# Performance work log

Measured on AMD Instinct MI355X. Metric: run time of the kernel, lower is better.

Reference implementation:

```python
import jax, jax.numpy as jnp
import numpy as np

N_RULES = 64  # R
OUT_PER_RULE = 64  # O, fc out = R*O = 4096


def setup_inputs() -> dict:
    key = jax.random.key(0)
    k1, k2, k3, k4 = jax.random.split(key, 4)
    S, D_IN = 8192, 1024
    RO = N_RULES * OUT_PER_RULE
    X = jax.random.normal(k1, (S, D_IN), dtype=jnp.float32)
    # torch.nn.Linear-style weight [out, in] and bias [out]
    W = jax.random.normal(k2, (RO, D_IN), dtype=jnp.float32) * (1.0 / np.sqrt(D_IN))
    b = jax.random.normal(k3, (RO,), dtype=jnp.float32) * 0.01
    # rule firing strengths (computed under no_grad in the original)
    lambdas = jax.random.uniform(k4, (S, N_RULES), dtype=jnp.float32)
    return {"X": X, "W": W, "b": b, "lambdas": lambdas}


def reference(X, W, b, lambdas):
    # fc + sigmoid: [S, R*O]
    H = jax.nn.sigmoid(X @ W.T + b)
    S = H.shape[0]
    # apply_rule_strength: block-diagonal lambda_eye @ H^T is exactly a
    # rule-weighted sum over the R consecutive O-sized blocks of H.
    Hr = H.reshape(S, N_RULES, OUT_PER_RULE)  # [S, R, O]
    Y = jnp.einsum("sr,sro->so", lambdas, Hr)  # [S, O]
    return Y
```

## Files before the change

### kernel.cpp

```cpp
#include <hip/hip_runtime.h>

#define S_DIM 8192
#define K_DIM 1024
#define RO_DIM 4096
#define O_DIM 64
#define SO (S_DIM * O_DIM)
#define NSLICE 16

typedef __attribute__((ext_vector_type(8))) __bf16 bf16x8;
typedef __attribute__((ext_vector_type(4))) float floatx4;
typedef __attribute__((ext_vector_type(4))) unsigned short ushx4;
typedef __attribute__((ext_vector_type(8))) unsigned short ushx8;

__device__ inline unsigned short f2bf(float f) {
  unsigned u = __builtin_bit_cast(unsigned, f);
  u += 0x7fff + ((u >> 16) & 1);
  return (unsigned short)(u >> 16);
}
__device__ inline float bf2f(unsigned short h) {
  unsigned u = ((unsigned)h) << 16;
  return __builtin_bit_cast(float, u);
}

__global__ __launch_bounds__(256) void cast_kernel(const float* __restrict__ X,
                                                   const float* __restrict__ W,
                                                   unsigned short* __restrict__ Xb,
                                                   unsigned short* __restrict__ Wb) {
  const int NX4 = (S_DIM * K_DIM) / 4;
#pragma unroll
  for (int i = 0; i < 4; ++i) {
    int g = blockIdx.x * 1024 + i * 256 + threadIdx.x;
    float4 v;
    unsigned short* dst;
    if (g < NX4) {
      v = ((const float4*)X)[g];
      dst = Xb + (size_t)g * 4;
    } else {
      int j = g - NX4;
      v = ((const float4*)W)[j];
      dst = Wb + (size_t)j * 4;
    }
    ushx4 o;
    o.x = f2bf(v.x); o.y = f2bf(v.y); o.z = f2bf(v.z); o.w = f2bf(v.w);
    *(ushx4*)dst = o;
  }
}


template <int MB, int NB>
__device__ __forceinline__ void mfmaq(floatx4 (&acc)[8][4], const bf16x8 (&afr)[4][2],
                                      const bf16x8 (&bfr)[4][2]) {
  __builtin_amdgcn_s_setprio(1);
#pragma unroll
  for (int ks = 0; ks < 2; ++ks)
#pragma unroll
    for (int m = 0; m < 4; ++m)
#pragma unroll
      for (int n = 0; n < 2; ++n)
        acc[MB + m][NB + n] = __builtin_amdgcn_mfma_f32_16x16x32_bf16(
            afr[m][ks], bfr[NB + n][ks], acc[MB + m][NB + n], 0, 0, 0);
  __builtin_amdgcn_s_setprio(0);
}

#define BAR() __builtin_amdgcn_s_barrier()

__global__ __launch_bounds__(512, 2) void gemm_kernel(const unsigned short* __restrict__ Xb,
                                                      const unsigned short* __restrict__ Wb,
                                                      const float* __restrict__ bias,
                                                      const float* __restrict__ lam,
                                                      unsigned short* __restrict__ partial) {
  __shared__ __align__(16) unsigned char smem[135168];
  unsigned short* sm = (unsigned short*)smem;
  float* lamsh = (float*)(smem + 131072);

  const int t = threadIdx.x;
  const int lane = t & 63;
  const int w = t >> 6;
  const int wm = w >> 2;
  const int wn = w & 3;
  const int quad = lane >> 4;
  const int l16 = lane & 15;

  int id = blockIdx.y * 16 + blockIdx.x;
  int x = id & 7;
  int j = id >> 3;
  const int bx = 2 * x + (j & 1);
  const int by = j >> 1;
  const int gm0 = by * 256;
  const int gn0 = bx * 256;

  const int rowt = t >> 3;
  const int gcc = (t & 7) ^ (rowt & 7);
  const size_t goff = (size_t)rowt * K_DIM + (size_t)gcc * 8;
  const unsigned short* Abase = Xb + (size_t)gm0 * K_DIM;
  const unsigned short* Bbase = Wb + (size_t)gn0 * K_DIM;

  auto STAGE = [&](const unsigned short* gbase, int half, int ktile, int slotOff) {
#pragma unroll
    for (int jj = 0; jj < 2; ++jj) {
      const unsigned short* src =
          gbase + (size_t)(half * 128 + jj * 64) * K_DIM + ktile * 64 + goff;
      __builtin_amdgcn_global_load_lds(
          (const __attribute__((address_space(1))) void*)src,
          (__attribute__((address_space(3))) void*)(sm + slotOff + jj * 4096 + t * 8),
          16, 0, 0);
    }
  };

  STAGE(Abase, 0, 0, 0);
  STAGE(Abase, 1, 0, 8192);
  STAGE(Bbase, 0, 0, 16384);
  STAGE(Bbase, 1, 0, 24576);
  STAGE(Bbase, 0, 1, 32768 + 16384);
  STAGE(Bbase, 1, 1, 32768 + 24576);
  STAGE(Abase, 0, 1, 32768 + 0);

  {
    int i = t;
    lamsh[i] = lam[(size_t)(gm0 + (i >> 2)) * 64 + bx * 4 + (i & 3)];
    i = t + 512;
    lamsh[i] = lam[(size_t)(gm0 + (i >> 2)) * 64 + bx * 4 + (i & 3)];
  }
  asm volatile("s_waitcnt vmcnt(6)" ::: "memory");
  BAR();

  floatx4 acc[8][4];
#pragma unroll
  for (int ni = 0; ni < 4; ++ni) {
    float bv = bias[gn0 + wn * 64 + ni * 16 + l16];
#pragma unroll
    for (int mi = 0; mi < 8; ++mi) acc[mi][ni] = (floatx4){bv, bv, bv, bv};
  }

  const int cA0 = ((quad) ^ (l16 & 7)) * 8;
  const int cA1 = ((4 + quad) ^ (l16 & 7)) * 8;

  for (int kt = 0; kt < 16; ++kt) {
    const int b = kt & 1;
    const unsigned short* As = sm + b * 32768 + wm * 8192 + l16 * 64;
    const unsigned short* Bs = sm + b * 32768 + 16384 + wn * 4096 + l16 * 64;
    const int bufN = (b ^ 1) * 32768;
    const int bufC = b * 32768;

    bf16x8 afr[4][2], bfr[4][2];

#pragma unroll
    for (int m = 0; m < 4; ++m) {
      afr[m][0] = *(const bf16x8*)(As + m * 1024 + cA0);
      afr[m][1] = *(const bf16x8*)(As + m * 1024 + cA1);
    }
#pragma unroll
    for (int n = 0; n < 2; ++n) {
      bfr[n][0] = *(const bf16x8*)(Bs + n * 1024 + cA0);
      bfr[n][1] = *(const bf16x8*)(Bs + n * 1024 + cA1);
    }
    if (kt < 15) STAGE(Abase, 1, kt + 1, bufN + 8192);
    BAR();
    mfmaq<0, 0>(acc, afr, bfr);
    BAR();

#pragma unroll
    for (int n = 2; n < 4; ++n) {
      bfr[n][0] = *(const bf16x8*)(Bs + n * 1024 + cA0);
      bfr[n][1] = *(const bf16x8*)(Bs + n * 1024 + cA1);
    }
    BAR();
    mfmaq<0, 2>(acc, afr, bfr);
    BAR();

#pragma unroll
    for (int m = 0; m < 4; ++m) {
      afr[m][0] = *(const bf16x8*)(As + (4 + m) * 1024 + cA0);
      afr[m][1] = *(const bf16x8*)(As + (4 + m) * 1024 + cA1);
    }
    if (kt < 14) STAGE(Bbase, 0, kt + 2, bufC + 16384);
    BAR();
    mfmaq<4, 0>(acc, afr, bfr);
    BAR();

    if (kt < 14) {
      STAGE(Bbase, 1, kt + 2, bufC + 24576);
      STAGE(Abase, 0, kt + 2, bufC + 0);
    }
    mfmaq<4, 2>(acc, afr, bfr);
    if (kt < 14) {
      asm volatile("s_waitcnt vmcnt(6)" ::: "memory");
    } else if (kt == 14) {
      asm volatile("s_waitcnt vmcnt(0)" ::: "memory");
    }
    BAR();
  }

  __syncthreads();
  {
    unsigned short* yreg = sm + wn * 16384;
#pragma unroll
    for (int mi = 0; mi < 8; ++mi) {
#pragma unroll
      for (int r = 0; r < 4; ++r) {
        int row = wm * 128 + mi * 16 + quad * 4 + r;
        float lamv = lamsh[row * 4 + wn];
#pragma unroll
        for (int ni = 0; ni < 4; ++ni) {
          float sg = 1.f / (1.f + __expf(-acc[mi][ni][r]));
          yreg[row * 64 + ((ni ^ quad) * 16) + l16] = f2bf(lamv * sg);
        }
      }
    }
  }
  __syncthreads();
  {
    unsigned short* pb = partial + (size_t)bx * SO + (size_t)gm0 * 64;
#pragma unroll
    for (int g = 0; g < 4; ++g) {
      int idx = g * 4096 + t * 8;
      int row = idx >> 6;
      int c = idx & 63;
      int phys = row * 64 + ((((c >> 4) ^ ((row >> 2) & 3))) << 4) + (c & 15);
      float s[8];
#pragma unroll
      for (int jj = 0; jj < 8; ++jj) s[jj] = 0.f;
#pragma unroll
      for (int q = 0; q < 4; ++q) {
        ushx8 v = *(const ushx8*)(sm + q * 16384 + phys);
#pragma unroll
        for (int jj = 0; jj < 8; ++jj) s[jj] += bf2f(v[jj]);
      }
      ushx8 o;
#pragma unroll
      for (int jj = 0; jj < 8; ++jj) o[jj] = f2bf(s[jj]);
      *(ushx8*)(pb + idx) = o;
    }
  }
}

__global__ __launch_bounds__(256) void reduce_kernel(const unsigned short* __restrict__ partial,
                                                     float* __restrict__ Y) {
  int i4 = blockIdx.x * 256 + threadIdx.x;
  float s0 = 0.f, s1 = 0.f, s2 = 0.f, s3 = 0.f;
#pragma unroll
  for (int c = 0; c < NSLICE; ++c) {
    ushx4 v = ((const ushx4*)(partial + (size_t)c * SO))[i4];
    s0 += bf2f(v.x); s1 += bf2f(v.y); s2 += bf2f(v.z); s3 += bf2f(v.w);
  }
  ((float4*)Y)[i4] = (float4){s0, s1, s2, s3};
}

extern "C" void kernel_launch(void* const* d_in, const int* in_sizes, int n_in,
                              void* d_out, int out_size, void* d_ws, size_t ws_size,
                              hipStream_t stream) {
  const float* X = (const float*)d_in[0];
  const float* W = (const float*)d_in[1];
  const float* b = (const float*)d_in[2];
  const float* lam = (const float*)d_in[3];
  float* Y = (float*)d_out;

  unsigned short* Xb = (unsigned short*)d_ws;
  unsigned short* Wb = Xb + (size_t)S_DIM * K_DIM;
  unsigned short* partial = Wb + (size_t)RO_DIM * K_DIM;

  int nCast = ((S_DIM + RO_DIM) * K_DIM / 4) / 1024;
  cast_kernel<<<nCast, 256, 0, stream>>>(X, W, Xb, Wb);

  dim3 g(RO_DIM / 256, S_DIM / 256);
  gemm_kernel<<<g, 512, 0, stream>>>(Xb, Wb, b, lam, partial);

  reduce_kernel<<<SO / 1024, 256, 0, stream>>>(partial, Y);
}
```

Measured before the change: 168.6 us.

## Prefetch next k-tile register fragments during final MFMA quadrant

Splits the A and B register fragments into separate double-buffered sets (af0/af1, bf01/bf23). The first A half and B columns 0-1 of the next k-tile are now read from LDS before the last MFMA quadrant of the current tile, and the global-to-LDS stage issues are regrouped around the quadrants. The aim is to hide LDS read latency behind MFMA work. In exchange it holds more live VGPRs under a 512-thread, 2-blocks-per-CU launch bound. It also reads the next buffer right after the waitcnt with no barrier first, so other threads' LDS writes may not be visible yet, and it adds one barrier per iteration.

```diff
diff --git a/kernel.cpp b/kernel.cpp
--- a/kernel.cpp
+++ b/kernel.cpp
@@ -48,8 +48,8 @@
 
 
 template <int MB, int NB>
-__device__ __forceinline__ void mfmaq(floatx4 (&acc)[8][4], const bf16x8 (&afr)[4][2],
-                                      const bf16x8 (&bfr)[4][2]) {
+__device__ __forceinline__ void mfmaq(floatx4 (&acc)[8][4], const bf16x8 (&af)[4][2],
+                                      const bf16x8 (&bf)[2][2]) {
   __builtin_amdgcn_s_setprio(1);
 #pragma unroll
   for (int ks = 0; ks < 2; ++ks)
@@ -58,8 +58,25 @@
 #pragma unroll
       for (int n = 0; n < 2; ++n)
         acc[MB + m][NB + n] = __builtin_amdgcn_mfma_f32_16x16x32_bf16(
-            afr[m][ks], bfr[NB + n][ks], acc[MB + m][NB + n], 0, 0, 0);
+            af[m][ks], bf[n][ks], acc[MB + m][NB + n], 0, 0, 0);
   __builtin_amdgcn_s_setprio(0);
+}
+
+__device__ __forceinline__ void rdA(bf16x8 (&af)[4][2], const unsigned short* As,
+                                    int mbase, int cA0, int cA1) {
+#pragma unroll
+  for (int m = 0; m < 4; ++m) {
+    af[m][0] = *(const bf16x8*)(As + (mbase + m) * 1024 + cA0);
+    af[m][1] = *(const bf16x8*)(As + (mbase + m) * 1024 + cA1);
+  }
+}
+__device__ __forceinline__ void rdB(bf16x8 (&bf)[2][2], const unsigned short* Bs,
+                                    int nbase, int cA0, int cA1) {
+#pragma unroll
+  for (int n = 0; n < 2; ++n) {
+    bf[n][0] = *(const bf16x8*)(Bs + (nbase + n) * 1024 + cA0);
+    bf[n][1] = *(const bf16x8*)(Bs + (nbase + n) * 1024 + cA1);
+  }
 }
 
 #define BAR() __builtin_amdgcn_s_barrier()
@@ -135,59 +152,52 @@
   const int cA0 = ((quad) ^ (l16 & 7)) * 8;
   const int cA1 = ((4 + quad) ^ (l16 & 7)) * 8;
 
+  const int Aoff = wm * 8192 + l16 * 64;
+  const int Boff = 16384 + wn * 4096 + l16 * 64;
+
+  bf16x8 af0[4][2], af1[4][2], bf01[2][2], bf23[2][2];
+
+  rdA(af0, sm + Aoff, 0, cA0, cA1);
+  rdB(bf01, sm + Boff, 0, cA0, cA1);
+
   for (int kt = 0; kt < 16; ++kt) {
     const int b = kt & 1;
-    const unsigned short* As = sm + b * 32768 + wm * 8192 + l16 * 64;
-    const unsigned short* Bs = sm + b * 32768 + 16384 + wn * 4096 + l16 * 64;
+    const unsigned short* As = sm + b * 32768 + Aoff;
+    const unsigned short* Bs = sm + b * 32768 + Boff;
+    const unsigned short* AsN = sm + (b ^ 1) * 32768 + Aoff;
+    const unsigned short* BsN = sm + (b ^ 1) * 32768 + Boff;
     const int bufN = (b ^ 1) * 32768;
     const int bufC = b * 32768;
 
-    bf16x8 afr[4][2], bfr[4][2];
-
-#pragma unroll
-    for (int m = 0; m < 4; ++m) {
-      afr[m][0] = *(const bf16x8*)(As + m * 1024 + cA0);
-      afr[m][1] = *(const bf16x8*)(As + m * 1024 + cA1);
-    }
-#pragma unroll
-    for (int n = 0; n < 2; ++n) {
-      bfr[n][0] = *(const bf16x8*)(Bs + n * 1024 + cA0);
-      bfr[n][1] = *(const bf16x8*)(Bs + n * 1024 + cA1);
-    }
+    rdB(bf23, Bs, 2, cA0, cA1);
     if (kt < 15) STAGE(Abase, 1, kt + 1, bufN + 8192);
     BAR();
-    mfmaq<0, 0>(acc, afr, bfr);
-    BAR();
-
-#pragma unroll
-    for (int n = 2; n < 4; ++n) {
-      bfr[n][0] = *(const bf16x8*)(Bs + n * 1024 + cA0);
-      bfr[n][1] = *(const bf16x8*)(Bs + n * 1024 + cA1);
-    }
-    BAR();
-    mfmaq<0, 2>(acc, afr, bfr);
-    BAR();
-
-#pragma unroll
-    for (int m = 0; m < 4; ++m) {
-      afr[m][0] = *(const bf16x8*)(As + (4 + m) * 1024 + cA0);
-      afr[m][1] = *(const bf16x8*)(As + (4 + m) * 1024 + cA1);
-    }
+    mfmaq<0, 0>(acc, af0, bf01);
+    BAR();
+
+    rdA(af1, As, 4, cA0, cA1);
     if (kt < 14) STAGE(Bbase, 0, kt + 2, bufC + 16384);
     BAR();
-    mfmaq<4, 0>(acc, afr, bfr);
+    mfmaq<0, 2>(acc, af0, bf23);
+    BAR();
+
+    if (kt < 14) STAGE(Bbase, 1, kt + 2, bufC + 24576);
+    BAR();
+    mfmaq<4, 0>(acc, af1, bf01);
     BAR();
 
     if (kt < 14) {
-      STAGE(Bbase, 1, kt + 2, bufC + 24576);
       STAGE(Abase, 0, kt + 2, bufC + 0);
-    }
-    mfmaq<4, 2>(acc, afr, bfr);
-    if (kt < 14) {
       asm volatile("s_waitcnt vmcnt(6)" ::: "memory");
     } else if (kt == 14) {
       asm volatile("s_waitcnt vmcnt(0)" ::: "memory");
     }
+    if (kt < 15) {
+      rdA(af0, AsN, 0, cA0, cA1);
+      rdB(bf01, BsN, 0, cA0, cA1);
+    }
+    BAR();
+    mfmaq<4, 2>(acc, af1, bf23);
     BAR();
   }
 
```

Result: no change. 166.3 us (-1.4%).

## Fuse fp32-to-bf16 cast into GEMM via register-staged loads

Applied to the files above, without the earlier changes.

Removes the separate cast kernel and makes the GEMM read fp32 X and W directly. Each tile is loaded into registers, converted with v_cvt_pk_bf16_f32, and written to LDS, replacing direct global-to-LDS loads. This saves the bf16 intermediate round trip and one launch. In exchange it doubles global read bytes per tile, since X and W are re-read as fp32 across tiles, and adds register pressure from the in-flight load sets. The pipeline now relies on the compiler's implicit vmcnt waits.

```diff
diff --git a/kernel.cpp b/kernel.cpp
--- a/kernel.cpp
+++ b/kernel.cpp
@@ -22,34 +22,16 @@
   return __builtin_bit_cast(float, u);
 }
 
-__global__ __launch_bounds__(256) void cast_kernel(const float* __restrict__ X,
-                                                   const float* __restrict__ W,
-                                                   unsigned short* __restrict__ Xb,
-                                                   unsigned short* __restrict__ Wb) {
-  const int NX4 = (S_DIM * K_DIM) / 4;
-#pragma unroll
-  for (int i = 0; i < 4; ++i) {
-    int g = blockIdx.x * 1024 + i * 256 + threadIdx.x;
-    float4 v;
-    unsigned short* dst;
-    if (g < NX4) {
-      v = ((const float4*)X)[g];
-      dst = Xb + (size_t)g * 4;
-    } else {
-      int j = g - NX4;
-      v = ((const float4*)W)[j];
-      dst = Wb + (size_t)j * 4;
-    }
-    ushx4 o;
-    o.x = f2bf(v.x); o.y = f2bf(v.y); o.z = f2bf(v.z); o.w = f2bf(v.w);
-    *(ushx4*)dst = o;
-  }
+__device__ __forceinline__ unsigned cvtpk(float lo, float hi) {
+  unsigned r;
+  asm("v_cvt_pk_bf16_f32 %0, %1, %2" : "=v"(r) : "v"(lo), "v"(hi));
+  return r;
 }
 
 
 template <int MB, int NB>
-__device__ __forceinline__ void mfmaq(floatx4 (&acc)[8][4], const bf16x8 (&afr)[4][2],
-                                      const bf16x8 (&bfr)[4][2]) {
+__device__ __forceinline__ void mfmaq(floatx4 (&acc)[8][4], const bf16x8 (&af)[4][2],
+                                      const bf16x8 (&bf)[4][2]) {
   __builtin_amdgcn_s_setprio(1);
 #pragma unroll
   for (int ks = 0; ks < 2; ++ks)
@@ -58,14 +40,16 @@
 #pragma unroll
       for (int n = 0; n < 2; ++n)
         acc[MB + m][NB + n] = __builtin_amdgcn_mfma_f32_16x16x32_bf16(
-            afr[m][ks], bfr[NB + n][ks], acc[MB + m][NB + n], 0, 0, 0);
+            af[m][ks], bf[NB + n][ks], acc[MB + m][NB + n], 0, 0, 0);
   __builtin_amdgcn_s_setprio(0);
 }
 
+struct ldset { float4 a, b, c, d; };
+
 #define BAR() __builtin_amdgcn_s_barrier()
 
-__global__ __launch_bounds__(512, 2) void gemm_kernel(const unsigned short* __restrict__ Xb,
-                                                      const unsigned short* __restrict__ Wb,
+__global__ __launch_bounds__(512, 2) void gemm_kernel(const float* __restrict__ X,
+                                                      const float* __restrict__ W,
                                                       const float* __restrict__ bias,
                                                       const float* __restrict__ lam,
                                                       unsigned short* __restrict__ partial) {
@@ -91,29 +75,35 @@
 
   const int rowt = t >> 3;
   const int gcc = (t & 7) ^ (rowt & 7);
-  const size_t goff = (size_t)rowt * K_DIM + (size_t)gcc * 8;
-  const unsigned short* Abase = Xb + (size_t)gm0 * K_DIM;
-  const unsigned short* Bbase = Wb + (size_t)gn0 * K_DIM;
-
-  auto STAGE = [&](const unsigned short* gbase, int half, int ktile, int slotOff) {
-#pragma unroll
-    for (int jj = 0; jj < 2; ++jj) {
-      const unsigned short* src =
-          gbase + (size_t)(half * 128 + jj * 64) * K_DIM + ktile * 64 + goff;
-      __builtin_amdgcn_global_load_lds(
-          (const __attribute__((address_space(1))) void*)src,
-          (__attribute__((address_space(3))) void*)(sm + slotOff + jj * 4096 + t * 8),
-          16, 0, 0);
-    }
+  const size_t goffE = (size_t)rowt * K_DIM + (size_t)gcc * 8;
+  const float* Asrc = X + (size_t)gm0 * K_DIM;
+  const float* Bsrc = W + (size_t)gn0 * K_DIM;
+
+  auto LDht = [&](ldset& h, const float* gb, int half, int ktile) {
+    const float* p0 = gb + (size_t)(half * 128) * K_DIM + ktile * 64 + goffE;
+    const float* p1 = p0 + (size_t)64 * K_DIM;
+    h.a = *(const float4*)p0; h.b = *(const float4*)(p0 + 4);
+    h.c = *(const float4*)p1; h.d = *(const float4*)(p1 + 4);
   };
-
-  STAGE(Abase, 0, 0, 0);
-  STAGE(Abase, 1, 0, 8192);
-  STAGE(Bbase, 0, 0, 16384);
-  STAGE(Bbase, 1, 0, 24576);
-  STAGE(Bbase, 0, 1, 32768 + 16384);
-  STAGE(Bbase, 1, 1, 32768 + 24576);
-  STAGE(Abase, 0, 1, 32768 + 0);
+  auto WRht = [&](const ldset& h, int slotOff) {
+    uint4 w0, w1;
+    w0.x = cvtpk(h.a.x, h.a.y); w0.y = cvtpk(h.a.z, h.a.w);
+    w0.z = cvtpk(h.b.x, h.b.y); w0.w = cvtpk(h.b.z, h.b.w);
+    w1.x = cvtpk(h.c.x, h.c.y); w1.y = cvtpk(h.c.z, h.c.w);
+    w1.z = cvtpk(h.d.x, h.d.y); w1.w = cvtpk(h.d.z, h.d.w);
+    *(uint4*)(sm + slotOff + t * 8) = w0;
+    *(uint4*)(sm + slotOff + 4096 + t * 8) = w1;
+  };
+
+  {
+    ldset u, v;
+    LDht(u, Asrc, 0, 0); LDht(v, Asrc, 1, 0); WRht(u, 0);              WRht(v, 8192);
+    LDht(u, Bsrc, 0, 0); LDht(v, Bsrc, 1, 0); WRht(u, 16384);          WRht(v, 24576);
+    LDht(u, Bsrc, 0, 1); LDht(v, Bsrc, 1, 1); WRht(u, 32768 + 16384);  WRht(v, 32768 + 24576);
+    LDht(u, Asrc, 0, 1); WRht(u, 32768 + 0);
+  }
+  ldset ldA1, ldB0, ldB1, ldA0;
+  LDht(ldA1, Asrc, 1, 1);
 
   {
     int i = t;
@@ -121,7 +111,7 @@
     i = t + 512;
     lamsh[i] = lam[(size_t)(gm0 + (i >> 2)) * 64 + bx * 4 + (i & 3)];
   }
-  asm volatile("s_waitcnt vmcnt(6)" ::: "memory");
+  asm volatile("s_waitcnt lgkmcnt(0)" ::: "memory");
   BAR();
 
   floatx4 acc[8][4];
@@ -154,9 +144,10 @@
       bfr[n][0] = *(const bf16x8*)(Bs + n * 1024 + cA0);
       bfr[n][1] = *(const bf16x8*)(Bs + n * 1024 + cA1);
     }
-    if (kt < 15) STAGE(Abase, 1, kt + 1, bufN + 8192);
+    if (kt < 15) WRht(ldA1, bufN + 8192);
     BAR();
     mfmaq<0, 0>(acc, afr, bfr);
+    if (kt < 14) LDht(ldB0, Bsrc, 0, kt + 2);
     BAR();
 
 #pragma unroll
@@ -166,6 +157,7 @@
     }
     BAR();
     mfmaq<0, 2>(acc, afr, bfr);
+    if (kt < 14) LDht(ldB1, Bsrc, 1, kt + 2);
     BAR();
 
 #pragma unroll
@@ -173,21 +165,19 @@
       afr[m][0] = *(const bf16x8*)(As + (4 + m) * 1024 + cA0);
       afr[m][1] = *(const bf16x8*)(As + (4 + m) * 1024 + cA1);
     }
-    if (kt < 14) STAGE(Bbase, 0, kt + 2, bufC + 16384);
+    if (kt < 14) WRht(ldB0, bufC + 16384);
     BAR();
     mfmaq<4, 0>(acc, afr, bfr);
+    if (kt < 14) LDht(ldA0, Asrc, 0, kt + 2);
     BAR();
 
     if (kt < 14) {
-      STAGE(Bbase, 1, kt + 2, bufC + 24576);
-      STAGE(Abase, 0, kt + 2, bufC + 0);
+      WRht(ldB1, bufC + 24576);
+      WRht(ldA0, bufC + 0);
     }
     mfmaq<4, 2>(acc, afr, bfr);
-    if (kt < 14) {
-      asm volatile("s_waitcnt vmcnt(6)" ::: "memory");
-    } else if (kt == 14) {
-      asm volatile("s_waitcnt vmcnt(0)" ::: "memory");
-    }
+    if (kt < 14) LDht(ldA1, Asrc, 1, kt + 2);
+    asm volatile("s_waitcnt lgkmcnt(0)" ::: "memory");
     BAR();
   }
 
@@ -255,15 +245,10 @@
   const float* lam = (const float*)d_in[3];
   float* Y = (float*)d_out;
 
-  unsigned short* Xb = (unsigned short*)d_ws;
-  unsigned short* Wb = Xb + (size_t)S_DIM * K_DIM;
-  unsigned short* partial = Wb + (size_t)RO_DIM * K_DIM;
-
-  int nCast = ((S_DIM + RO_DIM) * K_DIM / 4) / 1024;
-  cast_kernel<<<nCast, 256, 0, stream>>>(X, W, Xb, Wb);
+  unsigned short* partial = (unsigned short*)d_ws;
 
   dim3 g(RO_DIM / 256, S_DIM / 256);
-  gemm_kernel<<<g, 512, 0, stream>>>(Xb, Wb, b, lam, partial);
+  gemm_kernel<<<g, 512, 0, stream>>>(X, W, b, lam, partial);
 
   reduce_kernel<<<SO / 1024, 256, 0, stream>>>(partial, Y);
 }
```

After: 188.0 us. +11.5%, slower.

## Fuse slice reduction into GEMM via last-block atomic counter

Applied to the files above, without the earlier changes.

Removes the separate reduce kernel. Each GEMM block increments a per-row-block atomic counter after writing its bf16 partial, and the last of the 16 column blocks sums all slices for its 256 rows and writes Y directly. This saves one kernel launch and lets the reduction overlap with other blocks' GEMM work, at the cost of an added memset, thread fences, and serialized tail work in the last block per row group.

```diff
diff --git a/kernel.cpp b/kernel.cpp
--- a/kernel.cpp
+++ b/kernel.cpp
@@ -68,8 +68,11 @@
                                                       const unsigned short* __restrict__ Wb,
                                                       const float* __restrict__ bias,
                                                       const float* __restrict__ lam,
-                                                      unsigned short* __restrict__ partial) {
+                                                      unsigned short* __restrict__ partial,
+                                                      int* __restrict__ ctr,
+                                                      float* __restrict__ Y) {
   __shared__ __align__(16) unsigned char smem[135168];
+  __shared__ int lastFlag;
   unsigned short* sm = (unsigned short*)smem;
   float* lamsh = (float*)(smem + 131072);
 
@@ -232,18 +235,33 @@
       *(ushx8*)(pb + idx) = o;
     }
   }
-}
-
-__global__ __launch_bounds__(256) void reduce_kernel(const unsigned short* __restrict__ partial,
-                                                     float* __restrict__ Y) {
-  int i4 = blockIdx.x * 256 + threadIdx.x;
-  float s0 = 0.f, s1 = 0.f, s2 = 0.f, s3 = 0.f;
-#pragma unroll
-  for (int c = 0; c < NSLICE; ++c) {
-    ushx4 v = ((const ushx4*)(partial + (size_t)c * SO))[i4];
-    s0 += bf2f(v.x); s1 += bf2f(v.y); s2 += bf2f(v.z); s3 += bf2f(v.w);
-  }
-  ((float4*)Y)[i4] = (float4){s0, s1, s2, s3};
+
+  __syncthreads();
+  if (t == 0) {
+    __threadfence();
+    lastFlag = (atomicAdd(&ctr[by], 1) == NSLICE - 1);
+  }
+  __syncthreads();
+  if (lastFlag) {
+    __threadfence();
+    const unsigned short* pb0 = partial + (size_t)gm0 * 64;
+    float* Yb = Y + (size_t)gm0 * 64;
+#pragma unroll
+    for (int g = 0; g < 4; ++g) {
+      int idx = g * 4096 + t * 8;
+      float s[8];
+#pragma unroll
+      for (int jj = 0; jj < 8; ++jj) s[jj] = 0.f;
+#pragma unroll 4
+      for (int sl = 0; sl < NSLICE; ++sl) {
+        ushx8 v = *(const ushx8*)(pb0 + (size_t)sl * SO + idx);
+#pragma unroll
+        for (int jj = 0; jj < 8; ++jj) s[jj] += bf2f(v[jj]);
+      }
+      *(float4*)(Yb + idx) = (float4){s[0], s[1], s[2], s[3]};
+      *(float4*)(Yb + idx + 4) = (float4){s[4], s[5], s[6], s[7]};
+    }
+  }
 }
 
 extern "C" void kernel_launch(void* const* d_in, const int* in_sizes, int n_in,
@@ -258,12 +276,13 @@
   unsigned short* Xb = (unsigned short*)d_ws;
   unsigned short* Wb = Xb + (size_t)S_DIM * K_DIM;
   unsigned short* partial = Wb + (size_t)RO_DIM * K_DIM;
+  int* ctr = (int*)(partial + (size_t)NSLICE * SO);
+
+  hipMemsetAsync(ctr, 0, 32 * sizeof(int), stream);
 
   int nCast = ((S_DIM + RO_DIM) * K_DIM / 4) / 1024;
   cast_kernel<<<nCast, 256, 0, stream>>>(X, W, Xb, Wb);
 
   dim3 g(RO_DIM / 256, S_DIM / 256);
-  gemm_kernel<<<g, 512, 0, stream>>>(Xb, Wb, b, lam, partial);
-
-  reduce_kernel<<<SO / 1024, 256, 0, stream>>>(partial, Y);
-}
+  gemm_kernel<<<g, 512, 0, stream>>>(Xb, Wb, b, lam, partial, ctr, Y);
+}
```

Measured after the change: 234.8 us. 39.3% more time.
